# Performance work log

Hardware: AMD Instinct MI355X
Metric: run time of the kernel (lower is better)

Reference implementation:

```python
import jax, jax.numpy as jnp
import numpy as np

HIDDEN = 256   # HIDDEN_NUM
INPUT = 4      # fixed input_size
B, T = 128, 512


def _lstm_dir(xs, wi, wh, bi, bh):
    """Single-direction LSTM scan. xs: [T,B,D]; wi: [4H,D]; wh: [4H,H]; bi,bh: [4H].
    PyTorch gate order: i, f, g, o. Returns hidden states [T,B,H]."""
    Tn, Bn, _ = xs.shape
    Hn = wh.shape[1]
    # precompute input contribution for all timesteps (tiny D -> one big GEMM)
    gx = jnp.einsum('tbd,gd->tbg', xs, wi) + bi + bh  # [T,B,4H]

    def step(carry, g):
        h, c = carry
        g = g + h @ wh.T
        i, f, gg, o = jnp.split(g, 4, axis=-1)
        c = jax.nn.sigmoid(f) * c + jax.nn.sigmoid(i) * jnp.tanh(gg)
        h = jax.nn.sigmoid(o) * jnp.tanh(c)
        return (h, c), h

    init = (jnp.zeros((Bn, Hn), xs.dtype), jnp.zeros((Bn, Hn), xs.dtype))
    _, hs = jax.lax.scan(step, init, gx)
    return hs


def _lstm_bidir(xs, w_ih, w_hh, b_ih, b_hh):
    """xs: [T,B,D]; weights stacked over direction: w_ih [2,4H,D] etc. -> [T,B,2H]."""
    fwd = _lstm_dir(xs, w_ih[0], w_hh[0], b_ih[0], b_hh[0])
    bwd = _lstm_dir(xs[::-1], w_ih[1], w_hh[1], b_ih[1], b_hh[1])[::-1]
    return jnp.concatenate([fwd, bwd], axis=-1)


def setup_inputs() -> dict:
    key = jax.random.key(0)
    ks = jax.random.split(key, 12)
    k = 1.0 / np.sqrt(HIDDEN)
    u = lambda kk, shape: jax.random.uniform(kk, shape, jnp.float32, -k, k)
    H4 = 4 * HIDDEN
    return {
        'x': jax.random.normal(ks[0], (B, T, INPUT), jnp.float32),
        # layer 0 (input size 4), stacked [fwd, bwd]
        'w_ih0': u(ks[1], (2, H4, INPUT)),
        'w_hh0': u(ks[2], (2, H4, HIDDEN)),
        'b_ih0': u(ks[3], (2, H4)),
        'b_hh0': u(ks[4], (2, H4)),
        # layer 1 (input size 2H from bidirectional layer 0)
        'w_ih1': u(ks[5], (2, H4, 2 * HIDDEN)),
        'w_hh1': u(ks[6], (2, H4, HIDDEN)),
        'b_ih1': u(ks[7], (2, H4)),
        'b_hh1': u(ks[8], (2, H4)),
        # final linear: HIDDEN*2 -> 2
        'fc_w': u(ks[9], (2, 2 * HIDDEN)),
        'fc_b': u(ks[10], (2,)),
    }


def reference(x, w_ih0, w_hh0, b_ih0, b_hh0, w_ih1, w_hh1, b_ih1, b_hh1, fc_w, fc_b):
    xs = jnp.transpose(x, (1, 0, 2))                 # [T,B,4] (seq-major like torch)
    h0 = _lstm_bidir(xs, w_ih0, w_hh0, b_ih0, b_hh0)  # [T,B,2H]
    h1 = _lstm_bidir(h0, w_ih1, w_hh1, b_ih1, b_hh1)  # [T,B,2H]
    pooled = jnp.mean(h1, axis=0)                     # [B,2H]
    return pooled @ fc_w.T + fc_b                     # [B,2]
```

## Files before the change

kernel.cpp:

```cpp
#include <hip/hip_runtime.h>
#include <hip/hip_bf16.h>


typedef __bf16 bf16;
typedef __bf16 bf16x8 __attribute__((ext_vector_type(8)));
typedef float  f32x4  __attribute__((ext_vector_type(4)));
typedef unsigned int u32;
typedef unsigned long long u64;
typedef u64 u64x2 __attribute__((ext_vector_type(2)));

#define T_SEQ 512
#define BATCH 128
#define HID   256

#define H0_BYTES   67239936ULL
#define H1_BYTES   262144ULL
#define POOL_BYTES 262144ULL
#define FL0_OFF    (H0_BYTES + H1_BYTES + POOL_BYTES)
#define FL1_OFF    (FL0_OFF + 4096ULL)

#define MFMA16(a, b, c) __builtin_amdgcn_mfma_f32_16x16x32_bf16((a), (b), (c), 0, 0, 0)
#define AL(p)     __hip_atomic_load((p), __ATOMIC_RELAXED, __HIP_MEMORY_SCOPE_AGENT)
#define AS(p, v)  __hip_atomic_store((p), (v), __ATOMIC_RELAXED, __HIP_MEMORY_SCOPE_AGENT)

__device__ __forceinline__ float fsig(float v) {
    return __builtin_amdgcn_rcpf(1.0f + __expf(-v));
}
__device__ __forceinline__ float ftanh(float v) {
    float a = fabsf(v);
    float e = __expf(-2.0f * a);
    float r = (1.0f - e) * __builtin_amdgcn_rcpf(1.0f + e);
    return v < 0.0f ? -r : r;
}

__global__ void k_init(unsigned int* ws_u, int* flags0, int* flags1) {
    const int t = blockIdx.x * 256 + threadIdx.x;
    ws_u[t] = 0u;
    ws_u[(size_t)513 * 16384 + t] = 0u;
    unsigned int* h1u = ws_u + (H0_BYTES / 4);
    h1u[t] = 0u;
    h1u[32768 + t] = 0u;
    if (t < 1024) flags0[t] = 0;
    if (t < 2048) flags1[t] = 0;
}

__global__ __launch_bounds__(256, 1) void k_l0(
    const float* __restrict__ x, const float* __restrict__ wih,
    const float* __restrict__ whh, const float* __restrict__ bih,
    const float* __restrict__ bhh, bf16* __restrict__ h0,
    int* __restrict__ flags)
{
    __shared__ __align__(16) bf16 Hs[64][20];

    const int blk = blockIdx.x;
    const int dir = blk >> 5, bh = (blk >> 4) & 1, g = blk & 15;
    const int tid = threadIdx.x, wave = tid >> 6, lane = tid & 63;
    const int l15 = lane & 15, q = lane >> 4;
    const int j = g * 16 + l15;

    bf16x8 Bf[4][8];
#pragma unroll
    for (int tg = 0; tg < 4; ++tg) {
        const float* wr = whh + ((size_t)(dir * 1024 + tg * 256 + j)) * 256 + q * 8;
#pragma unroll
        for (int kt = 0; kt < 8; ++kt) {
            f32x4 aa = *(const f32x4*)(wr + kt * 32);
            f32x4 bb = *(const f32x4*)(wr + kt * 32 + 4);
            bf16x8 f;
            f[0] = (bf16)aa[0]; f[1] = (bf16)aa[1]; f[2] = (bf16)aa[2]; f[3] = (bf16)aa[3];
            f[4] = (bf16)bb[0]; f[5] = (bf16)bb[1]; f[6] = (bf16)bb[2]; f[7] = (bf16)bb[3];
            Bf[tg][kt] = f;
        }
    }
    float biasg[4], wx[4][4];
#pragma unroll
    for (int tg = 0; tg < 4; ++tg) {
        const int n = dir * 1024 + tg * 256 + j;
        biasg[tg] = bih[n] + bhh[n];
#pragma unroll
        for (int d2 = 0; d2 < 4; ++d2) wx[tg][d2] = wih[(size_t)n * 4 + d2];
    }

    float c4[4] = {0.f, 0.f, 0.f, 0.f};
    const int arow  = bh * 64 + wave * 16 + l15;
    const int lrow0 = wave * 16 + q * 4;
    const int mrow0 = bh * 64 + lrow0;
    const int srow = tid >> 2, scg = (tid & 3) * 4;
    int* fgrp = flags + (dir * 2 + bh) * 256;
    int budget = 30000000;

#pragma unroll 1
    for (int s = 1; s <= T_SEQ; ++s) {
        const int t_in = dir ? (T_SEQ - s) : (s - 1);

        f32x4 xv[4];
#pragma unroll
        for (int r = 0; r < 4; ++r)
            xv[r] = *(const f32x4*)(x + ((size_t)(mrow0 + r) * T_SEQ + t_in) * 4);
        f32x4 acc[4];
#pragma unroll
        for (int tg = 0; tg < 4; ++tg) {
#pragma unroll
            for (int r = 0; r < 4; ++r) {
                acc[tg][r] = biasg[tg] + xv[r][0] * wx[tg][0] + xv[r][1] * wx[tg][1]
                                       + xv[r][2] * wx[tg][2] + xv[r][3] * wx[tg][3];
            }
        }

        if (lane < 16) {
            const int need = s - 1;
            while (AL(fgrp + lane * 16) < need) {
                if (--budget < 0) break;
            }
        }
        asm volatile("" ::: "memory");

        const u64* hsrc = (const u64*)(h0 + ((size_t)(dir * 513 + (s - 1)) * BATCH + arow) * HID)
                          + q * 2;
        u64 av[16];
#pragma unroll
        for (int kt = 0; kt < 8; ++kt) {
            av[2 * kt]     = AL(hsrc + kt * 8);
            av[2 * kt + 1] = AL(hsrc + kt * 8 + 1);
        }
#pragma unroll
        for (int kt = 0; kt < 8; ++kt) {
            u64x2 t2; t2[0] = av[2 * kt]; t2[1] = av[2 * kt + 1];
            const bf16x8 A = __builtin_bit_cast(bf16x8, t2);
            acc[0] = MFMA16(A, Bf[0][kt], acc[0]);
            acc[1] = MFMA16(A, Bf[1][kt], acc[1]);
            acc[2] = MFMA16(A, Bf[2][kt], acc[2]);
            acc[3] = MFMA16(A, Bf[3][kt], acc[3]);
        }

#pragma unroll
        for (int r = 0; r < 4; ++r) {
            const float iv = fsig(acc[0][r]);
            const float fv = fsig(acc[1][r]);
            const float gv = ftanh(acc[2][r]);
            const float ov = fsig(acc[3][r]);
            c4[r] = fv * c4[r] + iv * gv;
            const float hv = ov * ftanh(c4[r]);
            Hs[lrow0 + r][l15] = (bf16)hv;
        }
        __syncthreads();
        {
            const u64 hv8 = *(const u64*)&Hs[srow][scg];
            u64* dst = (u64*)(h0 + ((size_t)(dir * 513 + s) * BATCH + bh * 64 + srow) * HID
                              + g * 16 + scg);
            AS(dst, hv8);
        }
        __syncthreads();
        if (tid == 0) AS(fgrp + g * 16, s);
    }
}

__global__ __launch_bounds__(256, 1) void k_l1(
    const float* __restrict__ wih1, const float* __restrict__ whh1,
    const float* __restrict__ bih1, const float* __restrict__ bhh1,
    bf16* __restrict__ h0, bf16* __restrict__ h1,
    float* __restrict__ pooled, int* __restrict__ flags)
{
    __shared__ float Gs[4][32][17];
    __shared__ __align__(16) bf16 Hs[32][20];
    __shared__ __align__(16) bf16 As1[32][264];

    const int blk = blockIdx.x;
    const int dir = blk >> 6, bq = (blk >> 4) & 3, g = blk & 15;
    const int tid = threadIdx.x, wave = tid >> 6, lane = tid & 63;
    const int l15 = lane & 15, q = lane >> 4;
    const int n = dir * 1024 + wave * 256 + g * 16 + l15;

    bf16x8 Bf[24];
#pragma unroll
    for (int kt = 0; kt < 24; ++kt) {
        const int k = kt * 32 + q * 8;
        const float* src = (kt < 8) ? (whh1 + (size_t)n * 256 + k)
                                    : (wih1 + (size_t)n * 512 + (k - 256));
        f32x4 aa = *(const f32x4*)src;
        f32x4 bb = *(const f32x4*)(src + 4);
        bf16x8 f;
        f[0] = (bf16)aa[0]; f[1] = (bf16)aa[1]; f[2] = (bf16)aa[2]; f[3] = (bf16)aa[3];
        f[4] = (bf16)bb[0]; f[5] = (bf16)bb[1]; f[6] = (bf16)bb[2]; f[7] = (bf16)bb[3];
        Bf[kt] = f;
    }
    const float biasw = bih1[n] + bhh1[n];
    const int r0 = tid >> 4, colu = tid & 15;
    float cst[2] = {0.f, 0.f}, pool[2] = {0.f, 0.f};
    int* fgrp = flags + (dir * 4 + bq) * 256;
    int budget = 30000000;

#pragma unroll 1
    for (int s = 1; s <= T_SEQ; ++s) {
        const int slotf = dir ? (513 - s) : s;
        const int slotb = dir ? s : (513 - s);

        f32x4 acc0 = {biasw, biasw, biasw, biasw};
        f32x4 acc1 = acc0;
        const bf16* f0 = h0 + ((size_t)slotf * BATCH + bq * 32 + l15) * HID + q * 8;
        const bf16* b0 = h0 + ((size_t)(513 + slotb) * BATCH + bq * 32 + l15) * HID + q * 8;
#pragma unroll
        for (int kt = 0; kt < 8; ++kt) {
            const bf16x8 af0 = *(const bf16x8*)(f0 + kt * 32);
            const bf16x8 af1 = *(const bf16x8*)(f0 + 16 * HID + kt * 32);
            acc0 = MFMA16(af0, Bf[8 + kt], acc0);
            acc1 = MFMA16(af1, Bf[8 + kt], acc1);
        }
#pragma unroll
        for (int kt = 0; kt < 8; ++kt) {
            const bf16x8 ab0 = *(const bf16x8*)(b0 + kt * 32);
            const bf16x8 ab1 = *(const bf16x8*)(b0 + 16 * HID + kt * 32);
            acc0 = MFMA16(ab0, Bf[16 + kt], acc0);
            acc1 = MFMA16(ab1, Bf[16 + kt], acc1);
        }

        if (lane < 16) {
            const int need = s - 1;
            while (AL(fgrp + lane * 16) < need) {
                if (--budget < 0) break;
            }
        }
        asm volatile("" ::: "memory");

        {
            const u64* hb = (const u64*)(h1 + ((size_t)(dir * 2 + ((s - 1) & 1)) * BATCH
                                               + bq * 32) * HID);
#pragma unroll
            for (int i = 0; i < 4; ++i) {
                const int chunk = tid + 256 * i;
                const int row = chunk >> 5, cc = chunk & 31;
                const u64* src = hb + (size_t)row * 32 + cc;
                const u64 lo = AL(hb + (size_t)row * 64 + cc * 2);
                const u64 hi = AL(hb + (size_t)row * 64 + cc * 2 + 1);
                (void)src;
                u64x2 t2; t2[0] = lo; t2[1] = hi;
                *(bf16x8*)(&As1[row][cc * 8]) = __builtin_bit_cast(bf16x8, t2);
            }
        }
        __syncthreads();

#pragma unroll
        for (int kt = 0; kt < 8; ++kt) {
            const bf16x8 a0 = *(const bf16x8*)(&As1[l15][kt * 32 + q * 8]);
            const bf16x8 a1 = *(const bf16x8*)(&As1[16 + l15][kt * 32 + q * 8]);
            acc0 = MFMA16(a0, Bf[kt], acc0);
            acc1 = MFMA16(a1, Bf[kt], acc1);
        }

#pragma unroll
        for (int r = 0; r < 4; ++r) {
            Gs[wave][q * 4 + r][l15]      = acc0[r];
            Gs[wave][16 + q * 4 + r][l15] = acc1[r];
        }
        __syncthreads();

#pragma unroll
        for (int rr = 0; rr < 2; ++rr) {
            const int r = r0 + rr * 16;
            const float iv = fsig(Gs[0][r][colu]);
            const float fv = fsig(Gs[1][r][colu]);
            const float gv = ftanh(Gs[2][r][colu]);
            const float ov = fsig(Gs[3][r][colu]);
            cst[rr] = fv * cst[rr] + iv * gv;
            const float hv = ov * ftanh(cst[rr]);
            pool[rr] += hv;
            Hs[r][colu] = (bf16)hv;
        }
        __syncthreads();
        {
            const int lrow = tid >> 3, c2 = (tid & 7) * 2;
            const u32 hv4 = *(const u32*)&Hs[lrow][c2];
            u32* dst = (u32*)(h1 + ((size_t)(dir * 2 + (s & 1)) * BATCH + bq * 32 + lrow) * HID
                              + g * 16 + c2);
            AS(dst, hv4);
        }
        __syncthreads();
        if (tid == 0) AS(fgrp + g * 16, s);
    }
#pragma unroll
    for (int rr = 0; rr < 2; ++rr) {
        const int r = r0 + rr * 16;
        pooled[((size_t)dir * BATCH + bq * 32 + r) * HID + g * 16 + colu] =
            pool[rr] * (1.0f / 512.0f);
    }
}

__global__ void k_fc(const float* __restrict__ pooled, const float* __restrict__ fcw,
                     const float* __restrict__ fcb, float* __restrict__ out)
{
    const int b = blockIdx.x;
    const int lane = threadIdx.x;
    float s0 = 0.f, s1 = 0.f;
#pragma unroll
    for (int jj = 0; jj < 8; ++jj) {
        const int jx = lane + jj * 64;
        const float p = (jx < 256) ? pooled[(size_t)b * 256 + jx]
                                   : pooled[32768 + (size_t)b * 256 + (jx - 256)];
        s0 += p * fcw[jx];
        s1 += p * fcw[512 + jx];
    }
#pragma unroll
    for (int off = 32; off > 0; off >>= 1) {
        s0 += __shfl_down(s0, off);
        s1 += __shfl_down(s1, off);
    }
    if (lane == 0) {
        out[b * 2 + 0] = s0 + fcb[0];
        out[b * 2 + 1] = s1 + fcb[1];
    }
}

extern "C" void kernel_launch(void* const* d_in, const int* in_sizes, int n_in,
                              void* d_out, int out_size, void* d_ws, size_t ws_size,
                              hipStream_t stream)
{
    const float* x    = (const float*)d_in[0];
    const float* wih0 = (const float*)d_in[1];
    const float* whh0 = (const float*)d_in[2];
    const float* bih0 = (const float*)d_in[3];
    const float* bhh0 = (const float*)d_in[4];
    const float* wih1 = (const float*)d_in[5];
    const float* whh1 = (const float*)d_in[6];
    const float* bih1 = (const float*)d_in[7];
    const float* bhh1 = (const float*)d_in[8];
    const float* fcw  = (const float*)d_in[9];
    const float* fcb  = (const float*)d_in[10];
    float* out = (float*)d_out;

    char* ws = (char*)d_ws;
    bf16* h0      = (bf16*)ws;
    bf16* h1      = (bf16*)(ws + H0_BYTES);
    float* pooled = (float*)(ws + H0_BYTES + H1_BYTES);
    int* flags0   = (int*)(ws + FL0_OFF);
    int* flags1   = (int*)(ws + FL1_OFF);

    k_init<<<dim3(64), dim3(256), 0, stream>>>((unsigned int*)ws, flags0, flags1);
    k_l0<<<dim3(64), dim3(256), 0, stream>>>(x, wih0, whh0, bih0, bhh0, h0, flags0);
    k_l1<<<dim3(128), dim3(256), 0, stream>>>(wih1, whh1, bih1, bhh1, h0, h1, pooled, flags1);
    k_fc<<<dim3(128), dim3(64), 0, stream>>>(pooled, fcw, fcb, out);
}
```

Before: 4.816 ms.

## Keep full layer-1 hidden history in ring buffer and load operands directly

When the workspace is large enough, layer 1 stores every timestep's hidden state in its own slot instead of a two-slot double buffer. It then feeds the MFMAs straight from global memory, dropping the LDS staging copy and one block barrier per step. Layer 0 likewise switches from relaxed atomic 64-bit loads to plain 128-bit vector loads of the previous hidden state. The spin-wait loops gain an s_sleep and a larger budget; the sleep may add wake-up latency on the serial critical path, and plain loads rely on fresh slots to avoid stale cached data.

New measurement: 5.845 ms. 1.21x slower.

```diff
diff --git a/kernel.cpp b/kernel.cpp
--- a/kernel.cpp
+++ b/kernel.cpp
@@ -14,10 +14,9 @@
 #define HID   256
 
 #define H0_BYTES   67239936ULL
-#define H1_BYTES   262144ULL
+#define H1R_BYTES  67239936ULL
+#define H1S_BYTES  262144ULL
 #define POOL_BYTES 262144ULL
-#define FL0_OFF    (H0_BYTES + H1_BYTES + POOL_BYTES)
-#define FL1_OFF    (FL0_OFF + 4096ULL)
 
 #define MFMA16(a, b, c) __builtin_amdgcn_mfma_f32_16x16x32_bf16((a), (b), (c), 0, 0, 0)
 #define AL(p)     __hip_atomic_load((p), __ATOMIC_RELAXED, __HIP_MEMORY_SCOPE_AGENT)
@@ -33,13 +32,18 @@
     return v < 0.0f ? -r : r;
 }
 
-__global__ void k_init(unsigned int* ws_u, int* flags0, int* flags1) {
+__global__ void k_init(unsigned int* ws_u, int* flags0, int* flags1, int ring) {
     const int t = blockIdx.x * 256 + threadIdx.x;
     ws_u[t] = 0u;
     ws_u[(size_t)513 * 16384 + t] = 0u;
     unsigned int* h1u = ws_u + (H0_BYTES / 4);
-    h1u[t] = 0u;
-    h1u[32768 + t] = 0u;
+    if (ring) {
+        h1u[t] = 0u;
+        h1u[(size_t)513 * 16384 + t] = 0u;
+    } else {
+        h1u[t] = 0u;
+        h1u[32768 + t] = 0u;
+    }
     if (t < 1024) flags0[t] = 0;
     if (t < 2048) flags1[t] = 0;
 }
@@ -87,7 +91,7 @@
     const int mrow0 = bh * 64 + lrow0;
     const int srow = tid >> 2, scg = (tid & 3) * 4;
     int* fgrp = flags + (dir * 2 + bh) * 256;
-    int budget = 30000000;
+    int budget = 200000000;
 
 #pragma unroll 1
     for (int s = 1; s <= T_SEQ; ++s) {
@@ -110,23 +114,16 @@
         if (lane < 16) {
             const int need = s - 1;
             while (AL(fgrp + lane * 16) < need) {
+                __builtin_amdgcn_s_sleep(1);
                 if (--budget < 0) break;
             }
         }
         asm volatile("" ::: "memory");
 
-        const u64* hsrc = (const u64*)(h0 + ((size_t)(dir * 513 + (s - 1)) * BATCH + arow) * HID)
-                          + q * 2;
-        u64 av[16];
+        const bf16* hsrc = h0 + ((size_t)(dir * 513 + (s - 1)) * BATCH + arow) * HID + q * 8;
 #pragma unroll
         for (int kt = 0; kt < 8; ++kt) {
-            av[2 * kt]     = AL(hsrc + kt * 8);
-            av[2 * kt + 1] = AL(hsrc + kt * 8 + 1);
-        }
-#pragma unroll
-        for (int kt = 0; kt < 8; ++kt) {
-            u64x2 t2; t2[0] = av[2 * kt]; t2[1] = av[2 * kt + 1];
-            const bf16x8 A = __builtin_bit_cast(bf16x8, t2);
+            const bf16x8 A = *(const bf16x8*)(hsrc + kt * 32);
             acc[0] = MFMA16(A, Bf[0][kt], acc[0]);
             acc[1] = MFMA16(A, Bf[1][kt], acc[1]);
             acc[2] = MFMA16(A, Bf[2][kt], acc[2]);
@@ -159,7 +156,7 @@
     const float* __restrict__ wih1, const float* __restrict__ whh1,
     const float* __restrict__ bih1, const float* __restrict__ bhh1,
     bf16* __restrict__ h0, bf16* __restrict__ h1,
-    float* __restrict__ pooled, int* __restrict__ flags)
+    float* __restrict__ pooled, int* __restrict__ flags, int ring)
 {
     __shared__ float Gs[4][32][17];
     __shared__ __align__(16) bf16 Hs[32][20];
@@ -188,7 +185,7 @@
     const int r0 = tid >> 4, colu = tid & 15;
     float cst[2] = {0.f, 0.f}, pool[2] = {0.f, 0.f};
     int* fgrp = flags + (dir * 4 + bq) * 256;
-    int budget = 30000000;
+    int budget = 200000000;
 
 #pragma unroll 1
     for (int s = 1; s <= T_SEQ; ++s) {
@@ -217,34 +214,41 @@
         if (lane < 16) {
             const int need = s - 1;
             while (AL(fgrp + lane * 16) < need) {
+                __builtin_amdgcn_s_sleep(1);
                 if (--budget < 0) break;
             }
         }
         asm volatile("" ::: "memory");
 
-        {
+        if (ring) {
+            const bf16* hb = h1 + ((size_t)(dir * 513 + (s - 1)) * BATCH + bq * 32) * HID;
+#pragma unroll
+            for (int kt = 0; kt < 8; ++kt) {
+                const bf16x8 a0 = *(const bf16x8*)(hb + (size_t)l15 * HID + kt * 32 + q * 8);
+                const bf16x8 a1 = *(const bf16x8*)(hb + (size_t)(16 + l15) * HID + kt * 32 + q * 8);
+                acc0 = MFMA16(a0, Bf[kt], acc0);
+                acc1 = MFMA16(a1, Bf[kt], acc1);
+            }
+        } else {
             const u64* hb = (const u64*)(h1 + ((size_t)(dir * 2 + ((s - 1) & 1)) * BATCH
                                                + bq * 32) * HID);
 #pragma unroll
             for (int i = 0; i < 4; ++i) {
                 const int chunk = tid + 256 * i;
                 const int row = chunk >> 5, cc = chunk & 31;
-                const u64* src = hb + (size_t)row * 32 + cc;
                 const u64 lo = AL(hb + (size_t)row * 64 + cc * 2);
                 const u64 hi = AL(hb + (size_t)row * 64 + cc * 2 + 1);
-                (void)src;
                 u64x2 t2; t2[0] = lo; t2[1] = hi;
                 *(bf16x8*)(&As1[row][cc * 8]) = __builtin_bit_cast(bf16x8, t2);
             }
-        }
-        __syncthreads();
-
-#pragma unroll
-        for (int kt = 0; kt < 8; ++kt) {
-            const bf16x8 a0 = *(const bf16x8*)(&As1[l15][kt * 32 + q * 8]);
-            const bf16x8 a1 = *(const bf16x8*)(&As1[16 + l15][kt * 32 + q * 8]);
-            acc0 = MFMA16(a0, Bf[kt], acc0);
-            acc1 = MFMA16(a1, Bf[kt], acc1);
+            __syncthreads();
+#pragma unroll
+            for (int kt = 0; kt < 8; ++kt) {
+                const bf16x8 a0 = *(const bf16x8*)(&As1[l15][kt * 32 + q * 8]);
+                const bf16x8 a1 = *(const bf16x8*)(&As1[16 + l15][kt * 32 + q * 8]);
+                acc0 = MFMA16(a0, Bf[kt], acc0);
+                acc1 = MFMA16(a1, Bf[kt], acc1);
+            }
         }
 
 #pragma unroll
@@ -270,8 +274,9 @@
         {
             const int lrow = tid >> 3, c2 = (tid & 7) * 2;
             const u32 hv4 = *(const u32*)&Hs[lrow][c2];
-            u32* dst = (u32*)(h1 + ((size_t)(dir * 2 + (s & 1)) * BATCH + bq * 32 + lrow) * HID
-                              + g * 16 + c2);
+            const size_t slot = ring ? ((size_t)(dir * 513 + s))
+                                     : ((size_t)(dir * 2 + (s & 1)));
+            u32* dst = (u32*)(h1 + (slot * BATCH + bq * 32 + lrow) * HID + g * 16 + c2);
             AS(dst, hv4);
         }
         __syncthreads();
@@ -327,15 +332,18 @@
     const float* fcb  = (const float*)d_in[10];
     float* out = (float*)d_out;
 
+    const int ring = (ws_size >= H0_BYTES + H1R_BYTES + POOL_BYTES + 16384ULL) ? 1 : 0;
+    const size_t h1b = ring ? H1R_BYTES : H1S_BYTES;
+
     char* ws = (char*)d_ws;
     bf16* h0      = (bf16*)ws;
     bf16* h1      = (bf16*)(ws + H0_BYTES);
-    float* pooled = (float*)(ws + H0_BYTES + H1_BYTES);
-    int* flags0   = (int*)(ws + FL0_OFF);
-    int* flags1   = (int*)(ws + FL1_OFF);
-
-    k_init<<<dim3(64), dim3(256), 0, stream>>>((unsigned int*)ws, flags0, flags1);
+    float* pooled = (float*)(ws + H0_BYTES + h1b);
+    int* flags0   = (int*)(ws + H0_BYTES + h1b + POOL_BYTES);
+    int* flags1   = flags0 + 1024;
+
+    k_init<<<dim3(64), dim3(256), 0, stream>>>((unsigned int*)ws, flags0, flags1, ring);
     k_l0<<<dim3(64), dim3(256), 0, stream>>>(x, wih0, whh0, bih0, bhh0, h0, flags0);
-    k_l1<<<dim3(128), dim3(256), 0, stream>>>(wih1, whh1, bih1, bhh1, h0, h1, pooled, flags1);
+    k_l1<<<dim3(128), dim3(256), 0, stream>>>(wih1, whh1, bih1, bhh1, h0, h1, pooled, flags1, ring);
     k_fc<<<dim3(128), dim3(64), 0, stream>>>(pooled, fcw, fcb, out);
 }
```

## Use per-wave flags and drop block barriers; restructure layer-1 LSTM blocks

Applied to the files above, without the earlier changes.

Each wave now writes its own slice of the hidden state and raises its own ready flag, so the __syncthreads barriers in the recurrent step are replaced by s_waitcnt waits. Layer 1 is rebuilt to match layer 0: 64 blocks where each wave computes all four gates for 16 batch rows in registers. This removes the shared-memory gate exchange and the cooperative staging of h1 into LDS. The layer-1 input weights are converted to bf16 by a new prep kernel and streamed from global memory every step instead of being held in registers, which trades register pressure and occupancy for extra memory traffic and twice as many flags to poll.

Result: slower. 5.752 ms (+19.4%).

```diff
diff --git a/kernel.cpp b/kernel.cpp
--- a/kernel.cpp
+++ b/kernel.cpp
@@ -3,6 +3,7 @@
 
 
 typedef __bf16 bf16;
+typedef __bf16 bf16x4 __attribute__((ext_vector_type(4)));
 typedef __bf16 bf16x8 __attribute__((ext_vector_type(8)));
 typedef float  f32x4  __attribute__((ext_vector_type(4)));
 typedef unsigned int u32;
@@ -14,10 +15,11 @@
 #define HID   256
 
 #define H0_BYTES   67239936ULL
-#define H1_BYTES   262144ULL
-#define POOL_BYTES 262144ULL
-#define FL0_OFF    (H0_BYTES + H1_BYTES + POOL_BYTES)
-#define FL1_OFF    (FL0_OFF + 4096ULL)
+#define H1_OFF     H0_BYTES
+#define POOL_OFF   (H1_OFF + 262144ULL)
+#define WIHB_OFF   (POOL_OFF + 262144ULL)
+#define FL0_OFF    (WIHB_OFF + 2097152ULL)
+#define FL1_OFF    (FL0_OFF + 16384ULL)
 
 #define MFMA16(a, b, c) __builtin_amdgcn_mfma_f32_16x16x32_bf16((a), (b), (c), 0, 0, 0)
 #define AL(p)     __hip_atomic_load((p), __ATOMIC_RELAXED, __HIP_MEMORY_SCOPE_AGENT)
@@ -37,11 +39,19 @@
     const int t = blockIdx.x * 256 + threadIdx.x;
     ws_u[t] = 0u;
     ws_u[(size_t)513 * 16384 + t] = 0u;
-    unsigned int* h1u = ws_u + (H0_BYTES / 4);
+    unsigned int* h1u = ws_u + (H1_OFF / 4);
     h1u[t] = 0u;
     h1u[32768 + t] = 0u;
-    if (t < 1024) flags0[t] = 0;
-    if (t < 2048) flags1[t] = 0;
+    if (t < 4096) flags0[t] = 0;
+    if (t < 4096) flags1[t] = 0;
+}
+
+__global__ void k_prep(const float* __restrict__ w, bf16* __restrict__ o) {
+    const int i = (blockIdx.x * 256 + threadIdx.x) * 4;
+    const f32x4 v = *(const f32x4*)(w + i);
+    bf16x4 r;
+    r[0] = (bf16)v[0]; r[1] = (bf16)v[1]; r[2] = (bf16)v[2]; r[3] = (bf16)v[3];
+    *(bf16x4*)(o + i) = r;
 }
 
 __global__ __launch_bounds__(256, 1) void k_l0(
@@ -50,7 +60,7 @@
     const float* __restrict__ bhh, bf16* __restrict__ h0,
     int* __restrict__ flags)
 {
-    __shared__ __align__(16) bf16 Hs[64][20];
+    __shared__ __align__(16) bf16 Hs[4][16][24];
 
     const int blk = blockIdx.x;
     const int dir = blk >> 5, bh = (blk >> 4) & 1, g = blk & 15;
@@ -83,11 +93,10 @@
 
     float c4[4] = {0.f, 0.f, 0.f, 0.f};
     const int arow  = bh * 64 + wave * 16 + l15;
-    const int lrow0 = wave * 16 + q * 4;
-    const int mrow0 = bh * 64 + lrow0;
-    const int srow = tid >> 2, scg = (tid & 3) * 4;
-    int* fgrp = flags + (dir * 2 + bh) * 256;
-    int budget = 30000000;
+    const int mrow0 = bh * 64 + wave * 16 + q * 4;
+    const int srow = lane >> 2, scg = (lane & 3) * 4;
+    int* fgrp = flags + (dir * 2 + bh) * 1024;
+    int budget = 100000000;
 
 #pragma unroll 1
     for (int s = 1; s <= T_SEQ; ++s) {
@@ -109,7 +118,7 @@
 
         if (lane < 16) {
             const int need = s - 1;
-            while (AL(fgrp + lane * 16) < need) {
+            while (AL(fgrp + (lane * 4 + wave) * 16) < need) {
                 if (--budget < 0) break;
             }
         }
@@ -141,147 +150,144 @@
             const float ov = fsig(acc[3][r]);
             c4[r] = fv * c4[r] + iv * gv;
             const float hv = ov * ftanh(c4[r]);
-            Hs[lrow0 + r][l15] = (bf16)hv;
-        }
-        __syncthreads();
+            Hs[wave][q * 4 + r][l15] = (bf16)hv;
+        }
+        asm volatile("s_waitcnt lgkmcnt(0)" ::: "memory");
         {
-            const u64 hv8 = *(const u64*)&Hs[srow][scg];
-            u64* dst = (u64*)(h0 + ((size_t)(dir * 513 + s) * BATCH + bh * 64 + srow) * HID
-                              + g * 16 + scg);
+            const u64 hv8 = *(const u64*)&Hs[wave][srow][scg];
+            u64* dst = (u64*)(h0 + ((size_t)(dir * 513 + s) * BATCH
+                              + bh * 64 + wave * 16 + srow) * HID + g * 16 + scg);
             AS(dst, hv8);
         }
-        __syncthreads();
-        if (tid == 0) AS(fgrp + g * 16, s);
+        asm volatile("s_waitcnt vmcnt(0)" ::: "memory");
+        if (lane == 0) AS(fgrp + (g * 4 + wave) * 16, s);
     }
 }
 
 __global__ __launch_bounds__(256, 1) void k_l1(
-    const float* __restrict__ wih1, const float* __restrict__ whh1,
-    const float* __restrict__ bih1, const float* __restrict__ bhh1,
+    const float* __restrict__ whh1, const float* __restrict__ bih1,
+    const float* __restrict__ bhh1, const bf16* __restrict__ wihb,
     bf16* __restrict__ h0, bf16* __restrict__ h1,
     float* __restrict__ pooled, int* __restrict__ flags)
 {
-    __shared__ float Gs[4][32][17];
-    __shared__ __align__(16) bf16 Hs[32][20];
-    __shared__ __align__(16) bf16 As1[32][264];
+    __shared__ __align__(16) bf16 Hs[4][16][24];
 
     const int blk = blockIdx.x;
-    const int dir = blk >> 6, bq = (blk >> 4) & 3, g = blk & 15;
+    const int dir = blk >> 5, bh = (blk >> 4) & 1, g = blk & 15;
     const int tid = threadIdx.x, wave = tid >> 6, lane = tid & 63;
     const int l15 = lane & 15, q = lane >> 4;
-    const int n = dir * 1024 + wave * 256 + g * 16 + l15;
-
-    bf16x8 Bf[24];
-#pragma unroll
-    for (int kt = 0; kt < 24; ++kt) {
-        const int k = kt * 32 + q * 8;
-        const float* src = (kt < 8) ? (whh1 + (size_t)n * 256 + k)
-                                    : (wih1 + (size_t)n * 512 + (k - 256));
-        f32x4 aa = *(const f32x4*)src;
-        f32x4 bb = *(const f32x4*)(src + 4);
-        bf16x8 f;
-        f[0] = (bf16)aa[0]; f[1] = (bf16)aa[1]; f[2] = (bf16)aa[2]; f[3] = (bf16)aa[3];
-        f[4] = (bf16)bb[0]; f[5] = (bf16)bb[1]; f[6] = (bf16)bb[2]; f[7] = (bf16)bb[3];
-        Bf[kt] = f;
-    }
-    const float biasw = bih1[n] + bhh1[n];
-    const int r0 = tid >> 4, colu = tid & 15;
-    float cst[2] = {0.f, 0.f}, pool[2] = {0.f, 0.f};
-    int* fgrp = flags + (dir * 4 + bq) * 256;
-    int budget = 30000000;
+    const int j = g * 16 + l15;
+
+    bf16x8 Bf[4][8];
+#pragma unroll
+    for (int tg = 0; tg < 4; ++tg) {
+        const float* wr = whh1 + ((size_t)(dir * 1024 + tg * 256 + j)) * 256 + q * 8;
+#pragma unroll
+        for (int kt = 0; kt < 8; ++kt) {
+            f32x4 aa = *(const f32x4*)(wr + kt * 32);
+            f32x4 bb = *(const f32x4*)(wr + kt * 32 + 4);
+            bf16x8 f;
+            f[0] = (bf16)aa[0]; f[1] = (bf16)aa[1]; f[2] = (bf16)aa[2]; f[3] = (bf16)aa[3];
+            f[4] = (bf16)bb[0]; f[5] = (bf16)bb[1]; f[6] = (bf16)bb[2]; f[7] = (bf16)bb[3];
+            Bf[tg][kt] = f;
+        }
+    }
+    float biasg[4];
+#pragma unroll
+    for (int tg = 0; tg < 4; ++tg) {
+        const int n = dir * 1024 + tg * 256 + j;
+        biasg[tg] = bih1[n] + bhh1[n];
+    }
+
+    float c4[4] = {0.f, 0.f, 0.f, 0.f};
+    float pool[4] = {0.f, 0.f, 0.f, 0.f};
+    const int arow = bh * 64 + wave * 16 + l15;
+    const int srow = lane >> 2, scg = (lane & 3) * 4;
+    const bf16* wb = wihb + ((size_t)(dir * 1024 + j)) * 512 + q * 8;
+    int* fgrp = flags + (dir * 2 + bh) * 1024;
+    int budget = 100000000;
 
 #pragma unroll 1
     for (int s = 1; s <= T_SEQ; ++s) {
         const int slotf = dir ? (513 - s) : s;
         const int slotb = dir ? s : (513 - s);
 
-        f32x4 acc0 = {biasw, biasw, biasw, biasw};
-        f32x4 acc1 = acc0;
-        const bf16* f0 = h0 + ((size_t)slotf * BATCH + bq * 32 + l15) * HID + q * 8;
-        const bf16* b0 = h0 + ((size_t)(513 + slotb) * BATCH + bq * 32 + l15) * HID + q * 8;
-#pragma unroll
-        for (int kt = 0; kt < 8; ++kt) {
-            const bf16x8 af0 = *(const bf16x8*)(f0 + kt * 32);
-            const bf16x8 af1 = *(const bf16x8*)(f0 + 16 * HID + kt * 32);
-            acc0 = MFMA16(af0, Bf[8 + kt], acc0);
-            acc1 = MFMA16(af1, Bf[8 + kt], acc1);
-        }
-#pragma unroll
-        for (int kt = 0; kt < 8; ++kt) {
-            const bf16x8 ab0 = *(const bf16x8*)(b0 + kt * 32);
-            const bf16x8 ab1 = *(const bf16x8*)(b0 + 16 * HID + kt * 32);
-            acc0 = MFMA16(ab0, Bf[16 + kt], acc0);
-            acc1 = MFMA16(ab1, Bf[16 + kt], acc1);
+        f32x4 acc[4];
+#pragma unroll
+        for (int tg = 0; tg < 4; ++tg) {
+            acc[tg][0] = biasg[tg]; acc[tg][1] = biasg[tg];
+            acc[tg][2] = biasg[tg]; acc[tg][3] = biasg[tg];
+        }
+        const bf16* af = h0 + ((size_t)slotf * BATCH + arow) * HID + q * 8;
+        const bf16* ab = h0 + ((size_t)(513 + slotb) * BATCH + arow) * HID + q * 8;
+#pragma unroll
+        for (int kt = 0; kt < 8; ++kt) {
+            const bf16x8 A = *(const bf16x8*)(af + kt * 32);
+            acc[0] = MFMA16(A, *(const bf16x8*)(wb + 0 * 131072 + kt * 32), acc[0]);
+            acc[1] = MFMA16(A, *(const bf16x8*)(wb + 1 * 131072 + kt * 32), acc[1]);
+            acc[2] = MFMA16(A, *(const bf16x8*)(wb + 2 * 131072 + kt * 32), acc[2]);
+            acc[3] = MFMA16(A, *(const bf16x8*)(wb + 3 * 131072 + kt * 32), acc[3]);
+        }
+#pragma unroll
+        for (int kt = 0; kt < 8; ++kt) {
+            const bf16x8 A = *(const bf16x8*)(ab + kt * 32);
+            acc[0] = MFMA16(A, *(const bf16x8*)(wb + 256 + 0 * 131072 + kt * 32), acc[0]);
+            acc[1] = MFMA16(A, *(const bf16x8*)(wb + 256 + 1 * 131072 + kt * 32), acc[1]);
+            acc[2] = MFMA16(A, *(const bf16x8*)(wb + 256 + 2 * 131072 + kt * 32), acc[2]);
+            acc[3] = MFMA16(A, *(const bf16x8*)(wb + 256 + 3 * 131072 + kt * 32), acc[3]);
         }
 
         if (lane < 16) {
             const int need = s - 1;
-            while (AL(fgrp + lane * 16) < need) {
+            while (AL(fgrp + (lane * 4 + wave) * 16) < need) {
                 if (--budget < 0) break;
             }
         }
         asm volatile("" ::: "memory");
 
+        const u64* hp = (const u64*)(h1 + ((size_t)(dir * 2 + ((s - 1) & 1)) * BATCH + arow) * HID)
+                        + q * 2;
+        u64 av[16];
+#pragma unroll
+        for (int kt = 0; kt < 8; ++kt) {
+            av[2 * kt]     = AL(hp + kt * 8);
+            av[2 * kt + 1] = AL(hp + kt * 8 + 1);
+        }
+#pragma unroll
+        for (int kt = 0; kt < 8; ++kt) {
+            u64x2 t2; t2[0] = av[2 * kt]; t2[1] = av[2 * kt + 1];
+            const bf16x8 A = __builtin_bit_cast(bf16x8, t2);
+            acc[0] = MFMA16(A, Bf[0][kt], acc[0]);
+            acc[1] = MFMA16(A, Bf[1][kt], acc[1]);
+            acc[2] = MFMA16(A, Bf[2][kt], acc[2]);
+            acc[3] = MFMA16(A, Bf[3][kt], acc[3]);
+        }
+
+#pragma unroll
+        for (int r = 0; r < 4; ++r) {
+            const float iv = fsig(acc[0][r]);
+            const float fv = fsig(acc[1][r]);
+            const float gv = ftanh(acc[2][r]);
+            const float ov = fsig(acc[3][r]);
+            c4[r] = fv * c4[r] + iv * gv;
+            const float hv = ov * ftanh(c4[r]);
+            pool[r] += hv;
+            Hs[wave][q * 4 + r][l15] = (bf16)hv;
+        }
+        asm volatile("s_waitcnt lgkmcnt(0)" ::: "memory");
         {
-            const u64* hb = (const u64*)(h1 + ((size_t)(dir * 2 + ((s - 1) & 1)) * BATCH
-                                               + bq * 32) * HID);
-#pragma unroll
-            for (int i = 0; i < 4; ++i) {
-                const int chunk = tid + 256 * i;
-                const int row = chunk >> 5, cc = chunk & 31;
-                const u64* src = hb + (size_t)row * 32 + cc;
-                const u64 lo = AL(hb + (size_t)row * 64 + cc * 2);
-                const u64 hi = AL(hb + (size_t)row * 64 + cc * 2 + 1);
-                (void)src;
-                u64x2 t2; t2[0] = lo; t2[1] = hi;
-                *(bf16x8*)(&As1[row][cc * 8]) = __builtin_bit_cast(bf16x8, t2);
-            }
-        }
-        __syncthreads();
-
-#pragma unroll
-        for (int kt = 0; kt < 8; ++kt) {
-            const bf16x8 a0 = *(const bf16x8*)(&As1[l15][kt * 32 + q * 8]);
-            const bf16x8 a1 = *(const bf16x8*)(&As1[16 + l15][kt * 32 + q * 8]);
-            acc0 = MFMA16(a0, Bf[kt], acc0);
-            acc1 = MFMA16(a1, Bf[kt], acc1);
-        }
-
-#pragma unroll
-        for (int r = 0; r < 4; ++r) {
-            Gs[wave][q * 4 + r][l15]      = acc0[r];
-            Gs[wave][16 + q * 4 + r][l15] = acc1[r];
-        }
-        __syncthreads();
-
-#pragma unroll
-        for (int rr = 0; rr < 2; ++rr) {
-            const int r = r0 + rr * 16;
-            const float iv = fsig(Gs[0][r][colu]);
-            const float fv = fsig(Gs[1][r][colu]);
-            const float gv = ftanh(Gs[2][r][colu]);
-            const float ov = fsig(Gs[3][r][colu]);
-            cst[rr] = fv * cst[rr] + iv * gv;
-            const float hv = ov * ftanh(cst[rr]);
-            pool[rr] += hv;
-            Hs[r][colu] = (bf16)hv;
-        }
-        __syncthreads();
-        {
-            const int lrow = tid >> 3, c2 = (tid & 7) * 2;
-            const u32 hv4 = *(const u32*)&Hs[lrow][c2];
-            u32* dst = (u32*)(h1 + ((size_t)(dir * 2 + (s & 1)) * BATCH + bq * 32 + lrow) * HID
-                              + g * 16 + c2);
-            AS(dst, hv4);
-        }
-        __syncthreads();
-        if (tid == 0) AS(fgrp + g * 16, s);
-    }
-#pragma unroll
-    for (int rr = 0; rr < 2; ++rr) {
-        const int r = r0 + rr * 16;
-        pooled[((size_t)dir * BATCH + bq * 32 + r) * HID + g * 16 + colu] =
-            pool[rr] * (1.0f / 512.0f);
+            const u64 hv8 = *(const u64*)&Hs[wave][srow][scg];
+            u64* dst = (u64*)(h1 + ((size_t)(dir * 2 + (s & 1)) * BATCH
+                              + bh * 64 + wave * 16 + srow) * HID + g * 16 + scg);
+            AS(dst, hv8);
+        }
+        asm volatile("s_waitcnt vmcnt(0)" ::: "memory");
+        if (lane == 0) AS(fgrp + (g * 4 + wave) * 16, s);
+    }
+#pragma unroll
+    for (int r = 0; r < 4; ++r) {
+        pooled[((size_t)dir * BATCH + bh * 64 + wave * 16 + q * 4 + r) * HID + j] =
+            pool[r] * (1.0f / 512.0f);
     }
 }
 
@@ -329,13 +335,15 @@
 
     char* ws = (char*)d_ws;
     bf16* h0      = (bf16*)ws;
-    bf16* h1      = (bf16*)(ws + H0_BYTES);
-    float* pooled = (float*)(ws + H0_BYTES + H1_BYTES);
+    bf16* h1      = (bf16*)(ws + H1_OFF);
+    float* pooled = (float*)(ws + POOL_OFF);
+    bf16* wihb    = (bf16*)(ws + WIHB_OFF);
     int* flags0   = (int*)(ws + FL0_OFF);
     int* flags1   = (int*)(ws + FL1_OFF);
 
     k_init<<<dim3(64), dim3(256), 0, stream>>>((unsigned int*)ws, flags0, flags1);
+    k_prep<<<dim3(1024), dim3(256), 0, stream>>>(wih1, wihb);
     k_l0<<<dim3(64), dim3(256), 0, stream>>>(x, wih0, whh0, bih0, bhh0, h0, flags0);
-    k_l1<<<dim3(128), dim3(256), 0, stream>>>(wih1, whh1, bih1, bhh1, h0, h1, pooled, flags1);
+    k_l1<<<dim3(64), dim3(256), 0, stream>>>(whh1, bih1, bhh1, wihb, h0, h1, pooled, flags1);
     k_fc<<<dim3(128), dim3(64), 0, stream>>>(pooled, fcw, fcb, out);
 }
```

## Replace flag-based cross-block sync with validity bits embedded in bf16 hidden states

Applied to the files above, without the earlier changes.

Removes the per-step flag arrays and the barriers around them. Each block now polls the hidden-state data directly, using the bf16 LSB as a ready marker: a set bit for layer 0's write-once slots, and a step-parity bit for layer 1's double buffer. Layer 1 loads the h0 inputs before polling, drops the LDS staging of h1, and double-buffers the gate scratch so only one barrier per step remains. This shortens the serial per-step critical path, but it perturbs the bf16 hidden values by one LSB and relies on 64-bit atomic loads observing whole stores.

Result: slower. 6.423 ms (+33.4%).

```diff
diff --git a/kernel.cpp b/kernel.cpp
--- a/kernel.cpp
+++ b/kernel.cpp
@@ -5,6 +5,7 @@
 typedef __bf16 bf16;
 typedef __bf16 bf16x8 __attribute__((ext_vector_type(8)));
 typedef float  f32x4  __attribute__((ext_vector_type(4)));
+typedef unsigned short u16;
 typedef unsigned int u32;
 typedef unsigned long long u64;
 typedef u64 u64x2 __attribute__((ext_vector_type(2)));
@@ -14,10 +15,10 @@
 #define HID   256
 
 #define H0_BYTES   67239936ULL
-#define H1_BYTES   262144ULL
-#define POOL_BYTES 262144ULL
-#define FL0_OFF    (H0_BYTES + H1_BYTES + POOL_BYTES)
-#define FL1_OFF    (FL0_OFF + 4096ULL)
+#define H1_OFF     H0_BYTES
+#define POOL_OFF   (H1_OFF + 262144ULL)
+
+#define LSBM 0x0001000100010001ULL
 
 #define MFMA16(a, b, c) __builtin_amdgcn_mfma_f32_16x16x32_bf16((a), (b), (c), 0, 0, 0)
 #define AL(p)     __hip_atomic_load((p), __ATOMIC_RELAXED, __HIP_MEMORY_SCOPE_AGENT)
@@ -32,25 +33,28 @@
     float r = (1.0f - e) * __builtin_amdgcn_rcpf(1.0f + e);
     return v < 0.0f ? -r : r;
 }
-
-__global__ void k_init(unsigned int* ws_u, int* flags0, int* flags1) {
+__device__ __forceinline__ bf16x8 mk_a(u64 lo, u64 hi) {
+    u64x2 t; t[0] = lo; t[1] = hi;
+    return __builtin_bit_cast(bf16x8, t);
+}
+
+__global__ void k_init(unsigned int* ws_u) {
     const int t = blockIdx.x * 256 + threadIdx.x;
-    ws_u[t] = 0u;
-    ws_u[(size_t)513 * 16384 + t] = 0u;
-    unsigned int* h1u = ws_u + (H0_BYTES / 4);
-    h1u[t] = 0u;
+    ws_u[t] = 0x00010001u;
+    ws_u[(size_t)513 * 16384 + t] = 0x00010001u;
+    unsigned int* h1u = ws_u + (H1_OFF / 4);
+    h1u[t]         = 0u;
+    h1u[16384 + t] = 0x00010001u;
     h1u[32768 + t] = 0u;
-    if (t < 1024) flags0[t] = 0;
-    if (t < 2048) flags1[t] = 0;
+    h1u[49152 + t] = 0x00010001u;
 }
 
 __global__ __launch_bounds__(256, 1) void k_l0(
     const float* __restrict__ x, const float* __restrict__ wih,
     const float* __restrict__ whh, const float* __restrict__ bih,
-    const float* __restrict__ bhh, bf16* __restrict__ h0,
-    int* __restrict__ flags)
+    const float* __restrict__ bhh, bf16* __restrict__ h0)
 {
-    __shared__ __align__(16) bf16 Hs[64][20];
+    __shared__ __align__(16) u16 Hs[4][16][24];
 
     const int blk = blockIdx.x;
     const int dir = blk >> 5, bh = (blk >> 4) & 1, g = blk & 15;
@@ -83,11 +87,8 @@
 
     float c4[4] = {0.f, 0.f, 0.f, 0.f};
     const int arow  = bh * 64 + wave * 16 + l15;
-    const int lrow0 = wave * 16 + q * 4;
-    const int mrow0 = bh * 64 + lrow0;
-    const int srow = tid >> 2, scg = (tid & 3) * 4;
-    int* fgrp = flags + (dir * 2 + bh) * 256;
-    int budget = 30000000;
+    const int mrow0 = bh * 64 + wave * 16 + q * 4;
+    const int srow = lane >> 2, scg = (lane & 3) * 4;
 
 #pragma unroll 1
     for (int s = 1; s <= T_SEQ; ++s) {
@@ -107,26 +108,26 @@
             }
         }
 
-        if (lane < 16) {
-            const int need = s - 1;
-            while (AL(fgrp + lane * 16) < need) {
-                if (--budget < 0) break;
-            }
-        }
-        asm volatile("" ::: "memory");
-
         const u64* hsrc = (const u64*)(h0 + ((size_t)(dir * 513 + (s - 1)) * BATCH + arow) * HID)
                           + q * 2;
         u64 av[16];
-#pragma unroll
-        for (int kt = 0; kt < 8; ++kt) {
-            av[2 * kt]     = AL(hsrc + kt * 8);
-            av[2 * kt + 1] = AL(hsrc + kt * 8 + 1);
-        }
-#pragma unroll
-        for (int kt = 0; kt < 8; ++kt) {
-            u64x2 t2; t2[0] = av[2 * kt]; t2[1] = av[2 * kt + 1];
-            const bf16x8 A = __builtin_bit_cast(bf16x8, t2);
+        {
+            unsigned pend = 0xffffu;
+            int rounds = 200000;
+            do {
+#pragma unroll
+                for (int c = 0; c < 16; ++c)
+                    if (pend & (1u << c)) av[c] = AL(hsrc + (c >> 1) * 8 + (c & 1));
+                unsigned np = 0;
+#pragma unroll
+                for (int c = 0; c < 16; ++c)
+                    if ((av[c] & LSBM) != LSBM) np |= (1u << c);
+                pend = np;
+            } while (pend && --rounds > 0);
+        }
+#pragma unroll
+        for (int kt = 0; kt < 8; ++kt) {
+            const bf16x8 A = mk_a(av[2 * kt], av[2 * kt + 1]);
             acc[0] = MFMA16(A, Bf[0][kt], acc[0]);
             acc[1] = MFMA16(A, Bf[1][kt], acc[1]);
             acc[2] = MFMA16(A, Bf[2][kt], acc[2]);
@@ -141,17 +142,16 @@
             const float ov = fsig(acc[3][r]);
             c4[r] = fv * c4[r] + iv * gv;
             const float hv = ov * ftanh(c4[r]);
-            Hs[lrow0 + r][l15] = (bf16)hv;
-        }
-        __syncthreads();
+            const u16 hb = (u16)(__builtin_bit_cast(u16, (bf16)hv) | 1u);
+            Hs[wave][q * 4 + r][l15] = hb;
+        }
+        asm volatile("s_waitcnt lgkmcnt(0)" ::: "memory");
         {
-            const u64 hv8 = *(const u64*)&Hs[srow][scg];
-            u64* dst = (u64*)(h0 + ((size_t)(dir * 513 + s) * BATCH + bh * 64 + srow) * HID
-                              + g * 16 + scg);
+            const u64 hv8 = *(const u64*)&Hs[wave][srow][scg];
+            u64* dst = (u64*)(h0 + ((size_t)(dir * 513 + s) * BATCH
+                              + bh * 64 + wave * 16 + srow) * HID + g * 16 + scg);
             AS(dst, hv8);
         }
-        __syncthreads();
-        if (tid == 0) AS(fgrp + g * 16, s);
     }
 }
 
@@ -159,11 +159,9 @@
     const float* __restrict__ wih1, const float* __restrict__ whh1,
     const float* __restrict__ bih1, const float* __restrict__ bhh1,
     bf16* __restrict__ h0, bf16* __restrict__ h1,
-    float* __restrict__ pooled, int* __restrict__ flags)
+    float* __restrict__ pooled)
 {
-    __shared__ float Gs[4][32][17];
-    __shared__ __align__(16) bf16 Hs[32][20];
-    __shared__ __align__(16) bf16 As1[32][264];
+    __shared__ float Gs[2][4][32][17];
 
     const int blk = blockIdx.x;
     const int dir = blk >> 6, bq = (blk >> 4) & 3, g = blk & 15;
@@ -187,95 +185,89 @@
     const float biasw = bih1[n] + bhh1[n];
     const int r0 = tid >> 4, colu = tid & 15;
     float cst[2] = {0.f, 0.f}, pool[2] = {0.f, 0.f};
-    int* fgrp = flags + (dir * 4 + bq) * 256;
-    int budget = 30000000;
+    u16* h1u = (u16*)h1;
 
 #pragma unroll 1
     for (int s = 1; s <= T_SEQ; ++s) {
         const int slotf = dir ? (513 - s) : s;
         const int slotb = dir ? s : (513 - s);
+        const int pb = s & 1;
+
+        const bf16* f0 = h0 + ((size_t)slotf * BATCH + bq * 32 + l15) * HID + q * 8;
+        const bf16* b0 = h0 + ((size_t)(513 + slotb) * BATCH + bq * 32 + l15) * HID + q * 8;
+        bf16x8 af0[8], af1[8], ab0[8], ab1[8];
+#pragma unroll
+        for (int kt = 0; kt < 8; ++kt) {
+            af0[kt] = *(const bf16x8*)(f0 + kt * 32);
+            af1[kt] = *(const bf16x8*)(f0 + 16 * HID + kt * 32);
+            ab0[kt] = *(const bf16x8*)(b0 + kt * 32);
+            ab1[kt] = *(const bf16x8*)(b0 + 16 * HID + kt * 32);
+        }
+
+        const u64 want = (((s - 1) >> 1) & 1) ? LSBM : 0ULL;
+        const u64* hp0 = (const u64*)(h1 + ((size_t)(dir * 2 + ((s - 1) & 1)) * BATCH
+                                            + bq * 32 + l15) * HID) + q * 2;
+        const u64* hp1 = hp0 + 16 * (HID / 4);
+        u64 av[32];
+        {
+            u32 pend = 0xffffffffu;
+            int rounds = 200000;
+            do {
+#pragma unroll
+                for (int c = 0; c < 16; ++c)
+                    if (pend & (1u << c)) av[c] = AL(hp0 + (c >> 1) * 8 + (c & 1));
+#pragma unroll
+                for (int c = 0; c < 16; ++c)
+                    if (pend & (1u << (16 + c))) av[16 + c] = AL(hp1 + (c >> 1) * 8 + (c & 1));
+                u32 np = 0;
+#pragma unroll
+                for (int c = 0; c < 32; ++c)
+                    if ((av[c] & LSBM) != want) np |= (1u << c);
+                pend = np;
+            } while (pend && --rounds > 0);
+        }
 
         f32x4 acc0 = {biasw, biasw, biasw, biasw};
         f32x4 acc1 = acc0;
-        const bf16* f0 = h0 + ((size_t)slotf * BATCH + bq * 32 + l15) * HID + q * 8;
-        const bf16* b0 = h0 + ((size_t)(513 + slotb) * BATCH + bq * 32 + l15) * HID + q * 8;
-#pragma unroll
-        for (int kt = 0; kt < 8; ++kt) {
-            const bf16x8 af0 = *(const bf16x8*)(f0 + kt * 32);
-            const bf16x8 af1 = *(const bf16x8*)(f0 + 16 * HID + kt * 32);
-            acc0 = MFMA16(af0, Bf[8 + kt], acc0);
-            acc1 = MFMA16(af1, Bf[8 + kt], acc1);
-        }
-#pragma unroll
-        for (int kt = 0; kt < 8; ++kt) {
-            const bf16x8 ab0 = *(const bf16x8*)(b0 + kt * 32);
-            const bf16x8 ab1 = *(const bf16x8*)(b0 + 16 * HID + kt * 32);
-            acc0 = MFMA16(ab0, Bf[16 + kt], acc0);
-            acc1 = MFMA16(ab1, Bf[16 + kt], acc1);
-        }
-
-        if (lane < 16) {
-            const int need = s - 1;
-            while (AL(fgrp + lane * 16) < need) {
-                if (--budget < 0) break;
-            }
-        }
-        asm volatile("" ::: "memory");
-
-        {
-            const u64* hb = (const u64*)(h1 + ((size_t)(dir * 2 + ((s - 1) & 1)) * BATCH
-                                               + bq * 32) * HID);
-#pragma unroll
-            for (int i = 0; i < 4; ++i) {
-                const int chunk = tid + 256 * i;
-                const int row = chunk >> 5, cc = chunk & 31;
-                const u64* src = hb + (size_t)row * 32 + cc;
-                const u64 lo = AL(hb + (size_t)row * 64 + cc * 2);
-                const u64 hi = AL(hb + (size_t)row * 64 + cc * 2 + 1);
-                (void)src;
-                u64x2 t2; t2[0] = lo; t2[1] = hi;
-                *(bf16x8*)(&As1[row][cc * 8]) = __builtin_bit_cast(bf16x8, t2);
-            }
+#pragma unroll
+        for (int kt = 0; kt < 8; ++kt) {
+            acc0 = MFMA16(af0[kt], Bf[8 + kt], acc0);
+            acc1 = MFMA16(af1[kt], Bf[8 + kt], acc1);
+        }
+#pragma unroll
+        for (int kt = 0; kt < 8; ++kt) {
+            acc0 = MFMA16(ab0[kt], Bf[16 + kt], acc0);
+            acc1 = MFMA16(ab1[kt], Bf[16 + kt], acc1);
+        }
+#pragma unroll
+        for (int kt = 0; kt < 8; ++kt) {
+            acc0 = MFMA16(mk_a(av[2 * kt], av[2 * kt + 1]), Bf[kt], acc0);
+            acc1 = MFMA16(mk_a(av[16 + 2 * kt], av[16 + 2 * kt + 1]), Bf[kt], acc1);
+        }
+
+#pragma unroll
+        for (int r = 0; r < 4; ++r) {
+            Gs[pb][wave][q * 4 + r][l15]      = acc0[r];
+            Gs[pb][wave][16 + q * 4 + r][l15] = acc1[r];
         }
         __syncthreads();
 
-#pragma unroll
-        for (int kt = 0; kt < 8; ++kt) {
-            const bf16x8 a0 = *(const bf16x8*)(&As1[l15][kt * 32 + q * 8]);
-            const bf16x8 a1 = *(const bf16x8*)(&As1[16 + l15][kt * 32 + q * 8]);
-            acc0 = MFMA16(a0, Bf[kt], acc0);
-            acc1 = MFMA16(a1, Bf[kt], acc1);
-        }
-
-#pragma unroll
-        for (int r = 0; r < 4; ++r) {
-            Gs[wave][q * 4 + r][l15]      = acc0[r];
-            Gs[wave][16 + q * 4 + r][l15] = acc1[r];
-        }
-        __syncthreads();
-
+        const u16 sbit = (u16)((s >> 1) & 1);
+        u16* hdst = h1u + ((size_t)(dir * 2 + (s & 1)) * BATCH + bq * 32) * HID + g * 16 + colu;
 #pragma unroll
         for (int rr = 0; rr < 2; ++rr) {
             const int r = r0 + rr * 16;
-            const float iv = fsig(Gs[0][r][colu]);
-            const float fv = fsig(Gs[1][r][colu]);
-            const float gv = ftanh(Gs[2][r][colu]);
-            const float ov = fsig(Gs[3][r][colu]);
+            const float iv = fsig(Gs[pb][0][r][colu]);
+            const float fv = fsig(Gs[pb][1][r][colu]);
+            const float gv = ftanh(Gs[pb][2][r][colu]);
+            const float ov = fsig(Gs[pb][3][r][colu]);
             cst[rr] = fv * cst[rr] + iv * gv;
             const float hv = ov * ftanh(cst[rr]);
             pool[rr] += hv;
-            Hs[r][colu] = (bf16)hv;
-        }
-        __syncthreads();
-        {
-            const int lrow = tid >> 3, c2 = (tid & 7) * 2;
-            const u32 hv4 = *(const u32*)&Hs[lrow][c2];
-            u32* dst = (u32*)(h1 + ((size_t)(dir * 2 + (s & 1)) * BATCH + bq * 32 + lrow) * HID
-                              + g * 16 + c2);
-            AS(dst, hv4);
-        }
-        __syncthreads();
-        if (tid == 0) AS(fgrp + g * 16, s);
+            u16 hb = __builtin_bit_cast(u16, (bf16)hv);
+            hb = (u16)((hb & 0xFFFEu) | sbit);
+            AS(hdst + (size_t)r * HID, hb);
+        }
     }
 #pragma unroll
     for (int rr = 0; rr < 2; ++rr) {
@@ -329,13 +321,11 @@
 
     char* ws = (char*)d_ws;
     bf16* h0      = (bf16*)ws;
-    bf16* h1      = (bf16*)(ws + H0_BYTES);
-    float* pooled = (float*)(ws + H0_BYTES + H1_BYTES);
-    int* flags0   = (int*)(ws + FL0_OFF);
-    int* flags1   = (int*)(ws + FL1_OFF);
-
-    k_init<<<dim3(64), dim3(256), 0, stream>>>((unsigned int*)ws, flags0, flags1);
-    k_l0<<<dim3(64), dim3(256), 0, stream>>>(x, wih0, whh0, bih0, bhh0, h0, flags0);
-    k_l1<<<dim3(128), dim3(256), 0, stream>>>(wih1, whh1, bih1, bhh1, h0, h1, pooled, flags1);
+    bf16* h1      = (bf16*)(ws + H1_OFF);
+    float* pooled = (float*)(ws + POOL_OFF);
+
+    k_init<<<dim3(64), dim3(256), 0, stream>>>((unsigned int*)ws);
+    k_l0<<<dim3(64), dim3(256), 0, stream>>>(x, wih0, whh0, bih0, bhh0, h0);
+    k_l1<<<dim3(128), dim3(256), 0, stream>>>(wih1, whh1, bih1, bhh1, h0, h1, pooled);
     k_fc<<<dim3(128), dim3(64), 0, stream>>>(pooled, fcw, fcb, out);
 }
```
